# Performance work log

Hardware: AMD Instinct MI355X
Metric: run time of the kernel (lower is better)

## Reference

```python
import jax, jax.numpy as jnp
import numpy as np

B, S, D, E, K = 4, 4096, 2048, 16, 2
TEMPERATURE = 1.0


def setup_inputs() -> dict:
    key = jax.random.key(0)
    ks = jax.random.split(key, 4)
    scale = 1.0 / np.sqrt(D)
    return {
        "x": jax.random.normal(ks[0], (B, S, D), dtype=jnp.float32),
        "w_route": jax.random.normal(ks[1], (D, E), dtype=jnp.float32) * scale,
        "b_route": jnp.zeros((E,), dtype=jnp.float32),
        "w_noise": jax.random.normal(ks[2], (D, E), dtype=jnp.float32) * scale,
        "b_noise": jnp.zeros((E,), dtype=jnp.float32),
        "eps": jax.random.normal(ks[3], (B, S, E), dtype=jnp.float32),
    }


def reference(x, w_route, b_route, w_noise, b_noise, eps):
    # dual linear projections: (B,S,D) @ (D,E) -> (B,S,E)
    logits = jnp.einsum("bsd,de->bse", x, w_route) + b_route
    noise_logits = jnp.einsum("bsd,de->bse", x, w_noise) + b_noise
    noise_scale = jax.nn.softplus(noise_logits)
    scaled_logits = (logits + eps * noise_scale) / TEMPERATURE

    top_k_logits, indices = jax.lax.top_k(scaled_logits, K)  # (B,S,K)
    # scatter top-k back over -inf, equivalent to masking non-topk entries
    in_topk = jax.nn.one_hot(indices, E, dtype=jnp.bool_).any(axis=-2)  # (B,S,E)
    sparse_logits = jnp.where(in_topk, scaled_logits, -jnp.inf)
    router_output = jax.nn.softmax(sparse_logits, axis=-1)

    router_prob = router_output.mean(axis=(0, 1))
    target = 1.0 / E
    aux_loss = jnp.sum((router_prob - target) ** 2)
    return router_output, indices, aux_loss
```

## Files before the change

### kernel.cpp

```cpp
#include <hip/hip_runtime.h>
#include <math.h>


#define DDIM 2048
#define NEXP 16
#define RPB 64
#define WAVE_D 256
#define NCHNK 16
#define IDX_OFF 262144
#define AUX_OFF 294912
#define NBLK 256

__global__ __launch_bounds__(512) void router_main_k(
    const float* __restrict__ x, const float* __restrict__ wr,
    const float* __restrict__ br, const float* __restrict__ wn,
    const float* __restrict__ bn, const float* __restrict__ eps,
    float* __restrict__ out, float* __restrict__ wsp) {
  __shared__ float smem[16384];

  const int tid  = threadIdx.x;
  const int wave = tid >> 6;
  const int lane = tid & 63;
  const int rg   = lane >> 3;
  const int q    = lane & 7;
  const int sw   = rg >> 1;
  const int row_base = blockIdx.x * RPB;

  float* xregion = smem + wave * 2048;

  const int srow  = lane >> 2;
  const int squad = lane & 3;
  const float* xsrc = x + (size_t)(row_base + srow) * DDIM + wave * WAVE_D + squad * 4;
  const int lwoff = srow * 16 + ((squad ^ ((srow >> 1) & 3)) << 2);

  const float* wbase = (q < 4 ? wr : wn) + (size_t)(wave * WAVE_D) * NEXP + (q & 3) * 4;

  float4 acc[8];
  #pragma unroll
  for (int i = 0; i < 8; ++i) acc[i] = make_float4(0.f, 0.f, 0.f, 0.f);

  float4 wp0[4], wp1[4];
  float4 xp[4];

  #pragma unroll
  for (int j = 0; j < 4; ++j) wp0[j] = *(const float4*)(wbase + j * NEXP);
  #pragma unroll
  for (int j = 0; j < 4; ++j) wp1[j] = *(const float4*)(wbase + 64 + j * NEXP);
  #pragma unroll
  for (int t = 0; t < 4; ++t) xp[t] = *(const float4*)(xsrc + (size_t)t * 16 * DDIM);
  #pragma unroll
  for (int t = 0; t < 4; ++t) *(float4*)(xregion + lwoff + t * 256) = xp[t];

#define FMA_ROW(WPA, GG, i) { \
    const float4 xv = *(const float4*)(xb + (rg + 8 * (i)) * 16 + (((GG) ^ sw) << 2)); \
    acc[i].x = fmaf(xv.w, WPA[3].x, fmaf(xv.z, WPA[2].x, fmaf(xv.y, WPA[1].x, fmaf(xv.x, WPA[0].x, acc[i].x)))); \
    acc[i].y = fmaf(xv.w, WPA[3].y, fmaf(xv.z, WPA[2].y, fmaf(xv.y, WPA[1].y, fmaf(xv.x, WPA[0].y, acc[i].y)))); \
    acc[i].z = fmaf(xv.w, WPA[3].z, fmaf(xv.z, WPA[2].z, fmaf(xv.y, WPA[1].z, fmaf(xv.x, WPA[0].z, acc[i].z)))); \
    acc[i].w = fmaf(xv.w, WPA[3].w, fmaf(xv.z, WPA[2].w, fmaf(xv.y, WPA[1].w, fmaf(xv.x, WPA[0].w, acc[i].w)))); }

  for (int k = 0; k < NCHNK; ++k) {
    const float* xb = xregion + (k & 1) * 1024;
    if (k + 1 < NCHNK) {
      #pragma unroll
      for (int t = 0; t < 4; ++t)
        xp[t] = *(const float4*)(xsrc + (size_t)t * 16 * DDIM + (k + 1) * 16);
    }
    #pragma unroll
    for (int i = 0; i < 8; ++i) FMA_ROW(wp0, 0, i);
    { const float* wl = wbase + (size_t)(4 * k + 2) * 64;
      #pragma unroll
      for (int j = 0; j < 4; ++j) wp0[j] = *(const float4*)(wl + j * NEXP); }
    #pragma unroll
    for (int i = 0; i < 8; ++i) FMA_ROW(wp1, 1, i);
    { const float* wl = wbase + (size_t)(4 * k + 3) * 64;
      #pragma unroll
      for (int j = 0; j < 4; ++j) wp1[j] = *(const float4*)(wl + j * NEXP); }
    #pragma unroll
    for (int i = 0; i < 8; ++i) FMA_ROW(wp0, 2, i);
    if (k + 1 < NCHNK) {
      const float* wl = wbase + (size_t)(4 * k + 4) * 64;
      #pragma unroll
      for (int j = 0; j < 4; ++j) wp0[j] = *(const float4*)(wl + j * NEXP);
    }
    #pragma unroll
    for (int i = 0; i < 8; ++i) FMA_ROW(wp1, 3, i);
    if (k + 1 < NCHNK) {
      const float* wl = wbase + (size_t)(4 * k + 5) * 64;
      #pragma unroll
      for (int j = 0; j < 4; ++j) wp1[j] = *(const float4*)(wl + j * NEXP);
      float* xw = xregion + ((k + 1) & 1) * 1024;
      #pragma unroll
      for (int t = 0; t < 4; ++t) *(float4*)(xw + lwoff + t * 256) = xp[t];
    }
  }

  const int psw = (q ^ rg) << 2;

#define DUMP_R(Rg) { float* pr = smem + (Rg) * 2048; \
    _Pragma("unroll") for (int i = 0; i < 8; ++i) \
      *(float4*)(pr + (rg + 8 * i) * 32 + psw) = acc[i]; }
#define ADD_R(Rg) { const float* pr = smem + (Rg) * 2048; \
    _Pragma("unroll") for (int i = 0; i < 8; ++i) { \
      float4 a = *(const float4*)(pr + (rg + 8 * i) * 32 + psw); \
      acc[i].x += a.x; acc[i].y += a.y; acc[i].z += a.z; acc[i].w += a.w; } }

  __syncthreads();
  if (wave >= 4) DUMP_R(wave - 4);
  __syncthreads();
  if (wave < 4)  ADD_R(wave);
  __syncthreads();
  if (wave >= 2 && wave < 4) DUMP_R(wave - 2);
  __syncthreads();
  if (wave < 2)  ADD_R(wave);
  __syncthreads();
  if (wave == 1) DUMP_R(0);
  __syncthreads();

  if (wave == 0) {
    ADD_R(0);
    DUMP_R(0);

    const int row_l = lane;
    const int row_g = row_base + row_l;
    float c[32];
    #pragma unroll
    for (int g = 0; g < 8; ++g) {
      float4 a = *(const float4*)(smem + row_l * 32 + ((g ^ (row_l & 7)) << 2));
      c[g * 4 + 0] = a.x; c[g * 4 + 1] = a.y; c[g * 4 + 2] = a.z; c[g * 4 + 3] = a.w;
    }

    float brv[16], bnv[16], ev[16];
    #pragma unroll
    for (int g = 0; g < 4; ++g) {
      *(float4*)(brv + g * 4) = *(const float4*)(br + g * 4);
      *(float4*)(bnv + g * 4) = *(const float4*)(bn + g * 4);
      *(float4*)(ev  + g * 4) = *(const float4*)(eps + (size_t)row_g * NEXP + g * 4);
    }

    float s[16];
    #pragma unroll
    for (int e = 0; e < 16; ++e) {
      float lg = c[e] + brv[e];
      float nz = c[16 + e] + bnv[e];
      float sp = fmaxf(nz, 0.f) + log1pf(expf(-fabsf(nz)));
      s[e] = lg + ev[e] * sp;
    }

    float b1 = s[0]; int i1 = 0;
    #pragma unroll
    for (int e = 1; e < 16; ++e) { if (s[e] > b1) { b1 = s[e]; i1 = e; } }
    float b2 = -INFINITY; int i2 = 0;
    #pragma unroll
    for (int e = 0; e < 16; ++e) { if (e != i1 && s[e] > b2) { b2 = s[e]; i2 = e; } }

    float t2 = expf(b2 - b1);
    float p1 = 1.f / (1.f + t2);
    float p2 = t2 / (1.f + t2);

    float v[16];
    #pragma unroll
    for (int e = 0; e < 16; ++e)
      v[e] = (e == i1) ? p1 : ((e == i2) ? p2 : 0.f);

    float* orow = out + (size_t)row_g * NEXP;
    *(float4*)(orow + 0)  = make_float4(v[0], v[1], v[2], v[3]);
    *(float4*)(orow + 4)  = make_float4(v[4], v[5], v[6], v[7]);
    *(float4*)(orow + 8)  = make_float4(v[8], v[9], v[10], v[11]);
    *(float4*)(orow + 12) = make_float4(v[12], v[13], v[14], v[15]);

    float* oidx = out + IDX_OFF + (size_t)row_g * 2;
    *(float2*)oidx = make_float2((float)i1, (float)i2);

    #pragma unroll
    for (int m = 1; m < 64; m <<= 1) {
      #pragma unroll
      for (int e = 0; e < 16; ++e) v[e] += __shfl_xor(v[e], m, 64);
    }
    if (lane == 0) {
      float* wpo = wsp + (size_t)blockIdx.x * 16;
      *(float4*)(wpo + 0)  = make_float4(v[0], v[1], v[2], v[3]);
      *(float4*)(wpo + 4)  = make_float4(v[4], v[5], v[6], v[7]);
      *(float4*)(wpo + 8)  = make_float4(v[8], v[9], v[10], v[11]);
      *(float4*)(wpo + 12) = make_float4(v[12], v[13], v[14], v[15]);
    }
  }
}

__global__ void router_aux_k(const float* __restrict__ wsp, float* __restrict__ out_aux) {
  __shared__ float red[16][17];
  __shared__ float sq[16];
  const int t = threadIdx.x;
  const int e = t & 15;
  const int g = t >> 4;
  float ssum = 0.f;
  #pragma unroll
  for (int b = 0; b < 16; ++b) ssum += wsp[(size_t)(g * 16 + b) * 16 + e];
  red[g][e] = ssum;
  __syncthreads();
  if (t < 16) {
    float tot = 0.f;
    #pragma unroll
    for (int gg = 0; gg < 16; ++gg) tot += red[gg][t];
    float diff = tot * (1.f / 16384.f) - 0.0625f;
    sq[t] = diff * diff;
  }
  __syncthreads();
  if (t == 0) {
    float a = 0.f;
    #pragma unroll
    for (int i = 0; i < 16; ++i) a += sq[i];
    *out_aux = a;
  }
}

extern "C" void kernel_launch(void* const* d_in, const int* in_sizes, int n_in,
                              void* d_out, int out_size, void* d_ws, size_t ws_size,
                              hipStream_t stream) {
  const float* x   = (const float*)d_in[0];
  const float* wr  = (const float*)d_in[1];
  const float* br  = (const float*)d_in[2];
  const float* wn  = (const float*)d_in[3];
  const float* bn  = (const float*)d_in[4];
  const float* eps = (const float*)d_in[5];
  float* out = (float*)d_out;
  float* wsp = (float*)d_ws;

  router_main_k<<<NBLK, 512, 0, stream>>>(x, wr, br, wn, bn, eps, out, wsp);
  router_aux_k<<<1, 256, 0, stream>>>(wsp, out + AUX_OFF);
}
```

Before: 52.02 us.

## Map one row per lane with wave-uniform scalar weight loads

Rewrites the per-wave matmul so each lane owns one row and all 32 expert outputs, reading its 16 x values from LDS and broadcasting the weights through wave-uniform (scalar) loads via readfirstlane. This removes the per-lane vector weight loads and the lane-group split of expert columns. The final transpose dump/reload in wave 0 also goes away because each lane already holds its row's logits. In exchange each lane keeps 32 accumulators, and the loop issues many scalar loads whose latency may not be hidden.

```diff
diff --git a/kernel.cpp b/kernel.cpp
--- a/kernel.cpp
+++ b/kernel.cpp
@@ -21,88 +21,75 @@
   const int tid  = threadIdx.x;
   const int wave = tid >> 6;
   const int lane = tid & 63;
-  const int rg   = lane >> 3;
-  const int q    = lane & 7;
-  const int sw   = rg >> 1;
+  const int wave_u = __builtin_amdgcn_readfirstlane(wave);
   const int row_base = blockIdx.x * RPB;
 
-  float* xregion = smem + wave * 2048;
+  float* xreg = smem + wave * 2048;
 
   const int srow  = lane >> 2;
   const int squad = lane & 3;
-  const float* xsrc = x + (size_t)(row_base + srow) * DDIM + wave * WAVE_D + squad * 4;
-  const int lwoff = srow * 16 + ((squad ^ ((srow >> 1) & 3)) << 2);
-
-  const float* wbase = (q < 4 ? wr : wn) + (size_t)(wave * WAVE_D) * NEXP + (q & 3) * 4;
-
-  float4 acc[8];
-  #pragma unroll
-  for (int i = 0; i < 8; ++i) acc[i] = make_float4(0.f, 0.f, 0.f, 0.f);
-
-  float4 wp0[4], wp1[4];
+  const float* xsrc = x + (size_t)(row_base + srow) * DDIM + wave_u * WAVE_D + squad * 4;
+  int woff[4];
+  #pragma unroll
+  for (int t = 0; t < 4; ++t) {
+    const int r = srow + 16 * t;
+    woff[t] = r * 16 + ((squad ^ ((r >> 3) & 3)) << 2);
+  }
+  const int rsw = (lane >> 3) & 3;
+
+  const float* wru = wr + (size_t)wave_u * WAVE_D * NEXP;
+  const float* wnu = wn + (size_t)wave_u * WAVE_D * NEXP;
+
+  float acc[32];
+  #pragma unroll
+  for (int e = 0; e < 32; ++e) acc[e] = 0.f;
+
   float4 xp[4];
-
-  #pragma unroll
-  for (int j = 0; j < 4; ++j) wp0[j] = *(const float4*)(wbase + j * NEXP);
-  #pragma unroll
-  for (int j = 0; j < 4; ++j) wp1[j] = *(const float4*)(wbase + 64 + j * NEXP);
   #pragma unroll
   for (int t = 0; t < 4; ++t) xp[t] = *(const float4*)(xsrc + (size_t)t * 16 * DDIM);
   #pragma unroll
-  for (int t = 0; t < 4; ++t) *(float4*)(xregion + lwoff + t * 256) = xp[t];
-
-#define FMA_ROW(WPA, GG, i) { \
-    const float4 xv = *(const float4*)(xb + (rg + 8 * (i)) * 16 + (((GG) ^ sw) << 2)); \
-    acc[i].x = fmaf(xv.w, WPA[3].x, fmaf(xv.z, WPA[2].x, fmaf(xv.y, WPA[1].x, fmaf(xv.x, WPA[0].x, acc[i].x)))); \
-    acc[i].y = fmaf(xv.w, WPA[3].y, fmaf(xv.z, WPA[2].y, fmaf(xv.y, WPA[1].y, fmaf(xv.x, WPA[0].y, acc[i].y)))); \
-    acc[i].z = fmaf(xv.w, WPA[3].z, fmaf(xv.z, WPA[2].z, fmaf(xv.y, WPA[1].z, fmaf(xv.x, WPA[0].z, acc[i].z)))); \
-    acc[i].w = fmaf(xv.w, WPA[3].w, fmaf(xv.z, WPA[2].w, fmaf(xv.y, WPA[1].w, fmaf(xv.x, WPA[0].w, acc[i].w)))); }
+  for (int t = 0; t < 4; ++t) *(float4*)(xreg + woff[t]) = xp[t];
 
   for (int k = 0; k < NCHNK; ++k) {
-    const float* xb = xregion + (k & 1) * 1024;
+    const float* xb = xreg + (k & 1) * 1024;
     if (k + 1 < NCHNK) {
       #pragma unroll
       for (int t = 0; t < 4; ++t)
         xp[t] = *(const float4*)(xsrc + (size_t)t * 16 * DDIM + (k + 1) * 16);
     }
-    #pragma unroll
-    for (int i = 0; i < 8; ++i) FMA_ROW(wp0, 0, i);
-    { const float* wl = wbase + (size_t)(4 * k + 2) * 64;
-      #pragma unroll
-      for (int j = 0; j < 4; ++j) wp0[j] = *(const float4*)(wl + j * NEXP); }
-    #pragma unroll
-    for (int i = 0; i < 8; ++i) FMA_ROW(wp1, 1, i);
-    { const float* wl = wbase + (size_t)(4 * k + 3) * 64;
-      #pragma unroll
-      for (int j = 0; j < 4; ++j) wp1[j] = *(const float4*)(wl + j * NEXP); }
-    #pragma unroll
-    for (int i = 0; i < 8; ++i) FMA_ROW(wp0, 2, i);
+    float xs[16];
+    #pragma unroll
+    for (int g = 0; g < 4; ++g)
+      *(float4*)(xs + 4 * g) = *(const float4*)(xb + lane * 16 + ((g ^ rsw) << 2));
+
+    const float* wRk = wru + (size_t)(k * 16) * NEXP;
+    const float* wNk = wnu + (size_t)(k * 16) * NEXP;
+    #pragma unroll
+    for (int d = 0; d < 16; ++d) {
+      const float xd = xs[d];
+      #pragma unroll
+      for (int e = 0; e < 16; ++e) {
+        acc[e]      = fmaf(xd, wRk[d * 16 + e], acc[e]);
+        acc[16 + e] = fmaf(xd, wNk[d * 16 + e], acc[16 + e]);
+      }
+    }
     if (k + 1 < NCHNK) {
-      const float* wl = wbase + (size_t)(4 * k + 4) * 64;
-      #pragma unroll
-      for (int j = 0; j < 4; ++j) wp0[j] = *(const float4*)(wl + j * NEXP);
-    }
-    #pragma unroll
-    for (int i = 0; i < 8; ++i) FMA_ROW(wp1, 3, i);
-    if (k + 1 < NCHNK) {
-      const float* wl = wbase + (size_t)(4 * k + 5) * 64;
-      #pragma unroll
-      for (int j = 0; j < 4; ++j) wp1[j] = *(const float4*)(wl + j * NEXP);
-      float* xw = xregion + ((k + 1) & 1) * 1024;
-      #pragma unroll
-      for (int t = 0; t < 4; ++t) *(float4*)(xw + lwoff + t * 256) = xp[t];
-    }
-  }
-
-  const int psw = (q ^ rg) << 2;
+      float* xw = xreg + ((k + 1) & 1) * 1024;
+      #pragma unroll
+      for (int t = 0; t < 4; ++t) *(float4*)(xw + woff[t]) = xp[t];
+    }
+  }
+
+  const int psw = (lane >> 2) & 7;
 
 #define DUMP_R(Rg) { float* pr = smem + (Rg) * 2048; \
-    _Pragma("unroll") for (int i = 0; i < 8; ++i) \
-      *(float4*)(pr + (rg + 8 * i) * 32 + psw) = acc[i]; }
+    _Pragma("unroll") for (int eq = 0; eq < 8; ++eq) \
+      *(float4*)(pr + lane * 32 + ((eq ^ psw) << 2)) = \
+        make_float4(acc[eq*4], acc[eq*4+1], acc[eq*4+2], acc[eq*4+3]); }
 #define ADD_R(Rg) { const float* pr = smem + (Rg) * 2048; \
-    _Pragma("unroll") for (int i = 0; i < 8; ++i) { \
-      float4 a = *(const float4*)(pr + (rg + 8 * i) * 32 + psw); \
-      acc[i].x += a.x; acc[i].y += a.y; acc[i].z += a.z; acc[i].w += a.w; } }
+    _Pragma("unroll") for (int eq = 0; eq < 8; ++eq) { \
+      float4 a = *(const float4*)(pr + lane * 32 + ((eq ^ psw) << 2)); \
+      acc[eq*4] += a.x; acc[eq*4+1] += a.y; acc[eq*4+2] += a.z; acc[eq*4+3] += a.w; } }
 
   __syncthreads();
   if (wave >= 4) DUMP_R(wave - 4);
@@ -118,16 +105,8 @@
 
   if (wave == 0) {
     ADD_R(0);
-    DUMP_R(0);
-
-    const int row_l = lane;
-    const int row_g = row_base + row_l;
-    float c[32];
-    #pragma unroll
-    for (int g = 0; g < 8; ++g) {
-      float4 a = *(const float4*)(smem + row_l * 32 + ((g ^ (row_l & 7)) << 2));
-      c[g * 4 + 0] = a.x; c[g * 4 + 1] = a.y; c[g * 4 + 2] = a.z; c[g * 4 + 3] = a.w;
-    }
+
+    const int row_g = row_base + lane;
 
     float brv[16], bnv[16], ev[16];
     #pragma unroll
@@ -140,8 +119,8 @@
     float s[16];
     #pragma unroll
     for (int e = 0; e < 16; ++e) {
-      float lg = c[e] + brv[e];
-      float nz = c[16 + e] + bnv[e];
+      float lg = acc[e] + brv[e];
+      float nz = acc[16 + e] + bnv[e];
       float sp = fmaxf(nz, 0.f) + log1pf(expf(-fabsf(nz)));
       s[e] = lg + ev[e] * sp;
     }
```

After: 76.92 us. 47.9% more time.

## Split the D reduction across blocks and move the epilogue into a separate kernel

Applied to the files above, without the earlier changes.

The old single kernel ran 256 blocks of 512 threads, each owning 64 rows over the full D. The new version splits D into NS slices across 1024 smaller 256-thread blocks, each writing partial sums to workspace. A new epilogue kernel then sums the slices and computes softmax, top-k and the aux partials. This is meant to raise occupancy and CU coverage on the memory-bound GEMV, at the cost of an extra kernel launch and partial-sum traffic through global memory, with a fallback that depends on workspace size.

```diff
diff --git a/kernel.cpp b/kernel.cpp
--- a/kernel.cpp
+++ b/kernel.cpp
@@ -4,19 +4,23 @@
 
 #define DDIM 2048
 #define NEXP 16
-#define RPB 64
-#define WAVE_D 256
-#define NCHNK 16
 #define IDX_OFF 262144
 #define AUX_OFF 294912
-#define NBLK 256
-
-__global__ __launch_bounds__(512) void router_main_k(
+
+#define FMA_ROW(WPA, GG, i) { \
+    const float4 xv = *(const float4*)(xb + (rg + 8 * (i)) * 16 + (((GG) ^ sw) << 2)); \
+    acc[i].x = fmaf(xv.w, WPA[3].x, fmaf(xv.z, WPA[2].x, fmaf(xv.y, WPA[1].x, fmaf(xv.x, WPA[0].x, acc[i].x)))); \
+    acc[i].y = fmaf(xv.w, WPA[3].y, fmaf(xv.z, WPA[2].y, fmaf(xv.y, WPA[1].y, fmaf(xv.x, WPA[0].y, acc[i].y)))); \
+    acc[i].z = fmaf(xv.w, WPA[3].z, fmaf(xv.z, WPA[2].z, fmaf(xv.y, WPA[1].z, fmaf(xv.x, WPA[0].z, acc[i].z)))); \
+    acc[i].w = fmaf(xv.w, WPA[3].w, fmaf(xv.z, WPA[2].w, fmaf(xv.y, WPA[1].w, fmaf(xv.x, WPA[0].w, acc[i].w)))); }
+
+template<int NS>
+__global__ __launch_bounds__(256) void gemv_k(
     const float* __restrict__ x, const float* __restrict__ wr,
-    const float* __restrict__ br, const float* __restrict__ wn,
-    const float* __restrict__ bn, const float* __restrict__ eps,
-    float* __restrict__ out, float* __restrict__ wsp) {
-  __shared__ float smem[16384];
+    const float* __restrict__ wn, float* __restrict__ pbase) {
+  constexpr int WAVE_DS = 512 / NS;
+  constexpr int NCHNK = WAVE_DS / 16;
+  __shared__ float smem[9216];
 
   const int tid  = threadIdx.x;
   const int wave = tid >> 6;
@@ -24,16 +28,19 @@
   const int rg   = lane >> 3;
   const int q    = lane & 7;
   const int sw   = rg >> 1;
-  const int row_base = blockIdx.x * RPB;
+  const int rowtile = blockIdx.x / NS;
+  const int dslice  = blockIdx.x % NS;
+  const int row_base = rowtile * 64;
+  const int d_base   = dslice * (DDIM / NS) + wave * WAVE_DS;
 
   float* xregion = smem + wave * 2048;
 
   const int srow  = lane >> 2;
   const int squad = lane & 3;
-  const float* xsrc = x + (size_t)(row_base + srow) * DDIM + wave * WAVE_D + squad * 4;
+  const float* xsrc = x + (size_t)(row_base + srow) * DDIM + d_base + squad * 4;
   const int lwoff = srow * 16 + ((squad ^ ((srow >> 1) & 3)) << 2);
 
-  const float* wbase = (q < 4 ? wr : wn) + (size_t)(wave * WAVE_D) * NEXP + (q & 3) * 4;
+  const float* wbase = (q < 4 ? wr : wn) + (size_t)d_base * NEXP + (q & 3) * 4;
 
   float4 acc[8];
   #pragma unroll
@@ -50,13 +57,6 @@
   for (int t = 0; t < 4; ++t) xp[t] = *(const float4*)(xsrc + (size_t)t * 16 * DDIM);
   #pragma unroll
   for (int t = 0; t < 4; ++t) *(float4*)(xregion + lwoff + t * 256) = xp[t];
-
-#define FMA_ROW(WPA, GG, i) { \
-    const float4 xv = *(const float4*)(xb + (rg + 8 * (i)) * 16 + (((GG) ^ sw) << 2)); \
-    acc[i].x = fmaf(xv.w, WPA[3].x, fmaf(xv.z, WPA[2].x, fmaf(xv.y, WPA[1].x, fmaf(xv.x, WPA[0].x, acc[i].x)))); \
-    acc[i].y = fmaf(xv.w, WPA[3].y, fmaf(xv.z, WPA[2].y, fmaf(xv.y, WPA[1].y, fmaf(xv.x, WPA[0].y, acc[i].y)))); \
-    acc[i].z = fmaf(xv.w, WPA[3].z, fmaf(xv.z, WPA[2].z, fmaf(xv.y, WPA[1].z, fmaf(xv.x, WPA[0].z, acc[i].z)))); \
-    acc[i].w = fmaf(xv.w, WPA[3].w, fmaf(xv.z, WPA[2].w, fmaf(xv.y, WPA[1].w, fmaf(xv.x, WPA[0].w, acc[i].w)))); }
 
   for (int k = 0; k < NCHNK; ++k) {
     const float* xb = xregion + (k & 1) * 1024;
@@ -94,99 +94,112 @@
     }
   }
 
-  const int psw = (q ^ rg) << 2;
-
-#define DUMP_R(Rg) { float* pr = smem + (Rg) * 2048; \
-    _Pragma("unroll") for (int i = 0; i < 8; ++i) \
-      *(float4*)(pr + (rg + 8 * i) * 32 + psw) = acc[i]; }
-#define ADD_R(Rg) { const float* pr = smem + (Rg) * 2048; \
-    _Pragma("unroll") for (int i = 0; i < 8; ++i) { \
-      float4 a = *(const float4*)(pr + (rg + 8 * i) * 32 + psw); \
-      acc[i].x += a.x; acc[i].y += a.y; acc[i].z += a.z; acc[i].w += a.w; } }
-
+  {
+    float* pr = xregion;
+    const int psw = (q ^ rg) << 2;
+    #pragma unroll
+    for (int i = 0; i < 8; ++i)
+      *(float4*)(pr + (rg + 8 * i) * 32 + psw) = acc[i];
+  }
   __syncthreads();
-  if (wave >= 4) DUMP_R(wave - 4);
-  __syncthreads();
-  if (wave < 4)  ADD_R(wave);
-  __syncthreads();
-  if (wave >= 2 && wave < 4) DUMP_R(wave - 2);
-  __syncthreads();
-  if (wave < 2)  ADD_R(wave);
-  __syncthreads();
-  if (wave == 1) DUMP_R(0);
-  __syncthreads();
-
-  if (wave == 0) {
-    ADD_R(0);
-    DUMP_R(0);
-
-    const int row_l = lane;
-    const int row_g = row_base + row_l;
-    float c[32];
-    #pragma unroll
-    for (int g = 0; g < 8; ++g) {
-      float4 a = *(const float4*)(smem + row_l * 32 + ((g ^ (row_l & 7)) << 2));
-      c[g * 4 + 0] = a.x; c[g * 4 + 1] = a.y; c[g * 4 + 2] = a.z; c[g * 4 + 3] = a.w;
-    }
-
-    float brv[16], bnv[16], ev[16];
-    #pragma unroll
-    for (int g = 0; g < 4; ++g) {
-      *(float4*)(brv + g * 4) = *(const float4*)(br + g * 4);
-      *(float4*)(bnv + g * 4) = *(const float4*)(bn + g * 4);
-      *(float4*)(ev  + g * 4) = *(const float4*)(eps + (size_t)row_g * NEXP + g * 4);
-    }
-
-    float s[16];
-    #pragma unroll
-    for (int e = 0; e < 16; ++e) {
-      float lg = c[e] + brv[e];
-      float nz = c[16 + e] + bnv[e];
-      float sp = fmaxf(nz, 0.f) + log1pf(expf(-fabsf(nz)));
-      s[e] = lg + ev[e] * sp;
-    }
-
-    float b1 = s[0]; int i1 = 0;
-    #pragma unroll
-    for (int e = 1; e < 16; ++e) { if (s[e] > b1) { b1 = s[e]; i1 = e; } }
-    float b2 = -INFINITY; int i2 = 0;
-    #pragma unroll
-    for (int e = 0; e < 16; ++e) { if (e != i1 && s[e] > b2) { b2 = s[e]; i2 = e; } }
-
-    float t2 = expf(b2 - b1);
-    float p1 = 1.f / (1.f + t2);
-    float p2 = t2 / (1.f + t2);
-
-    float v[16];
-    #pragma unroll
-    for (int e = 0; e < 16; ++e)
-      v[e] = (e == i1) ? p1 : ((e == i2) ? p2 : 0.f);
-
-    float* orow = out + (size_t)row_g * NEXP;
-    *(float4*)(orow + 0)  = make_float4(v[0], v[1], v[2], v[3]);
-    *(float4*)(orow + 4)  = make_float4(v[4], v[5], v[6], v[7]);
-    *(float4*)(orow + 8)  = make_float4(v[8], v[9], v[10], v[11]);
-    *(float4*)(orow + 12) = make_float4(v[12], v[13], v[14], v[15]);
-
-    float* oidx = out + IDX_OFF + (size_t)row_g * 2;
-    *(float2*)oidx = make_float2((float)i1, (float)i2);
-
-    #pragma unroll
-    for (int m = 1; m < 64; m <<= 1) {
-      #pragma unroll
-      for (int e = 0; e < 16; ++e) v[e] += __shfl_xor(v[e], m, 64);
-    }
-    if (lane == 0) {
-      float* wpo = wsp + (size_t)blockIdx.x * 16;
-      *(float4*)(wpo + 0)  = make_float4(v[0], v[1], v[2], v[3]);
-      *(float4*)(wpo + 4)  = make_float4(v[4], v[5], v[6], v[7]);
-      *(float4*)(wpo + 8)  = make_float4(v[8], v[9], v[10], v[11]);
-      *(float4*)(wpo + 12) = make_float4(v[12], v[13], v[14], v[15]);
-    }
-  }
-}
-
-__global__ void router_aux_k(const float* __restrict__ wsp, float* __restrict__ out_aux) {
+
+  float* pws = pbase + (size_t)(dslice * 256 + rowtile) * 2048;
+  #pragma unroll
+  for (int u = 0; u < 2; ++u) {
+    const int f   = tid * 2 + u;
+    const int row = f >> 3;
+    const int g   = f & 7;
+    const int off = row * 32 + ((g ^ (row & 7)) << 2);
+    float4 a0 = *(const float4*)(smem + 0 * 2048 + off);
+    float4 a1 = *(const float4*)(smem + 1 * 2048 + off);
+    float4 a2 = *(const float4*)(smem + 2 * 2048 + off);
+    float4 a3 = *(const float4*)(smem + 3 * 2048 + off);
+    float4 s = make_float4((a0.x + a1.x) + (a2.x + a3.x),
+                           (a0.y + a1.y) + (a2.y + a3.y),
+                           (a0.z + a1.z) + (a2.z + a3.z),
+                           (a0.w + a1.w) + (a2.w + a3.w));
+    *(float4*)(pws + row * 32 + g * 4) = s;
+  }
+}
+
+template<int NS>
+__global__ __launch_bounds__(64) void epi_k(
+    const float* __restrict__ pbase, const float* __restrict__ br,
+    const float* __restrict__ bn, const float* __restrict__ eps,
+    float* __restrict__ out, float* __restrict__ auxs) {
+  const int lane = threadIdx.x;
+  const int bid  = blockIdx.x;
+  const int row_g = bid * 64 + lane;
+
+  float c[32];
+  #pragma unroll
+  for (int g = 0; g < 8; ++g) {
+    float4 a = make_float4(0.f, 0.f, 0.f, 0.f);
+    #pragma unroll
+    for (int s = 0; s < NS; ++s) {
+      float4 p = *(const float4*)(pbase + (size_t)(s * 256 + bid) * 2048 + lane * 32 + g * 4);
+      a.x += p.x; a.y += p.y; a.z += p.z; a.w += p.w;
+    }
+    c[g * 4 + 0] = a.x; c[g * 4 + 1] = a.y; c[g * 4 + 2] = a.z; c[g * 4 + 3] = a.w;
+  }
+
+  float brv[16], bnv[16], ev[16];
+  #pragma unroll
+  for (int g = 0; g < 4; ++g) {
+    *(float4*)(brv + g * 4) = *(const float4*)(br + g * 4);
+    *(float4*)(bnv + g * 4) = *(const float4*)(bn + g * 4);
+    *(float4*)(ev  + g * 4) = *(const float4*)(eps + (size_t)row_g * NEXP + g * 4);
+  }
+
+  float s[16];
+  #pragma unroll
+  for (int e = 0; e < 16; ++e) {
+    float lg = c[e] + brv[e];
+    float nz = c[16 + e] + bnv[e];
+    float sp = fmaxf(nz, 0.f) + log1pf(expf(-fabsf(nz)));
+    s[e] = lg + ev[e] * sp;
+  }
+
+  float b1 = s[0]; int i1 = 0;
+  #pragma unroll
+  for (int e = 1; e < 16; ++e) { if (s[e] > b1) { b1 = s[e]; i1 = e; } }
+  float b2 = -INFINITY; int i2 = 0;
+  #pragma unroll
+  for (int e = 0; e < 16; ++e) { if (e != i1 && s[e] > b2) { b2 = s[e]; i2 = e; } }
+
+  float t2 = expf(b2 - b1);
+  float p1 = 1.f / (1.f + t2);
+  float p2 = t2 / (1.f + t2);
+
+  float v[16];
+  #pragma unroll
+  for (int e = 0; e < 16; ++e)
+    v[e] = (e == i1) ? p1 : ((e == i2) ? p2 : 0.f);
+
+  float* orow = out + (size_t)row_g * NEXP;
+  *(float4*)(orow + 0)  = make_float4(v[0], v[1], v[2], v[3]);
+  *(float4*)(orow + 4)  = make_float4(v[4], v[5], v[6], v[7]);
+  *(float4*)(orow + 8)  = make_float4(v[8], v[9], v[10], v[11]);
+  *(float4*)(orow + 12) = make_float4(v[12], v[13], v[14], v[15]);
+
+  float* oidx = out + IDX_OFF + (size_t)row_g * 2;
+  *(float2*)oidx = make_float2((float)i1, (float)i2);
+
+  #pragma unroll
+  for (int m = 1; m < 64; m <<= 1) {
+    #pragma unroll
+    for (int e = 0; e < 16; ++e) v[e] += __shfl_xor(v[e], m, 64);
+  }
+  if (lane == 0) {
+    float* ap = auxs + (size_t)bid * 16;
+    *(float4*)(ap + 0)  = make_float4(v[0], v[1], v[2], v[3]);
+    *(float4*)(ap + 4)  = make_float4(v[4], v[5], v[6], v[7]);
+    *(float4*)(ap + 8)  = make_float4(v[8], v[9], v[10], v[11]);
+    *(float4*)(ap + 12) = make_float4(v[12], v[13], v[14], v[15]);
+  }
+}
+
+__global__ void router_aux_k(const float* __restrict__ auxs, float* __restrict__ out_aux) {
   __shared__ float red[16][17];
   __shared__ float sq[16];
   const int t = threadIdx.x;
@@ -194,7 +207,7 @@
   const int g = t >> 4;
   float ssum = 0.f;
   #pragma unroll
-  for (int b = 0; b < 16; ++b) ssum += wsp[(size_t)(g * 16 + b) * 16 + e];
+  for (int b = 0; b < 16; ++b) ssum += auxs[(size_t)(g * 16 + b) * 16 + e];
   red[g][e] = ssum;
   __syncthreads();
   if (t < 16) {
@@ -223,8 +236,23 @@
   const float* bn  = (const float*)d_in[4];
   const float* eps = (const float*)d_in[5];
   float* out = (float*)d_out;
-  float* wsp = (float*)d_ws;
-
-  router_main_k<<<NBLK, 512, 0, stream>>>(x, wr, br, wn, bn, eps, out, wsp);
-  router_aux_k<<<1, 256, 0, stream>>>(wsp, out + AUX_OFF);
-}
+
+  float* wsf   = (float*)d_ws;
+  float* auxs  = wsf;
+  float* pbase = wsf + 4096;
+
+  const size_t need4 = (size_t)(4096 + 4 * 524288) * 4;
+  const size_t need2 = (size_t)(4096 + 2 * 524288) * 4;
+
+  if (ws_size >= need4) {
+    gemv_k<4><<<1024, 256, 0, stream>>>(x, wr, wn, pbase);
+    epi_k<4><<<256, 64, 0, stream>>>(pbase, br, bn, eps, out, auxs);
+  } else if (ws_size >= need2) {
+    gemv_k<2><<<512, 256, 0, stream>>>(x, wr, wn, pbase);
+    epi_k<2><<<256, 64, 0, stream>>>(pbase, br, bn, eps, out, auxs);
+  } else {
+    gemv_k<1><<<256, 256, 0, stream>>>(x, wr, wn, pbase);
+    epi_k<1><<<256, 64, 0, stream>>>(pbase, br, bn, eps, out, auxs);
+  }
+  router_aux_k<<<1, 256, 0, stream>>>(auxs, out + AUX_OFF);
+}
```

After: 60.68 us. 1.17x slower.
